# Kernel tuning notes

Measured on AMD Instinct MI355X. Metric: run time of the kernel, lower is better.

The kernel has to match this reference:

```python
import jax, jax.numpy as jnp
import numpy as np

CIN = 256
WINDOWS = (2, 4, 6)
LN_EPS = 1e-5


def _conv1x1(x, w, b):
    # x: (N,C,H,W), w: (O,C), b: (O,)
    return jnp.einsum('nchw,oc->nohw', x, w) + b[None, :, None, None]


def _pos_encoding(C, H, W):
    # Faithful to SinCosPositionalEncoding2D (incl. its w-major flatten + raw view)
    gw, gh = jnp.meshgrid(jnp.arange(W, dtype=jnp.float32),
                          jnp.arange(H, dtype=jnp.float32), indexing='ij')
    pd = C // 4
    omega = 1.0 / (10000.0 ** (jnp.arange(pd, dtype=jnp.float32) / pd))
    ow = gw.reshape(-1)[:, None] * omega[None, :]
    oh = gh.reshape(-1)[:, None] * omega[None, :]
    pe = jnp.concatenate([jnp.sin(ow), jnp.cos(ow), jnp.sin(oh), jnp.cos(oh)], axis=1)  # (W*H, C)
    return pe.reshape(1, C, H, W)  # raw row-major reinterpret, matching torch .view


def _unfold(x, kh, kw, sh, sw):
    # torch F.unfold semantics: (N,C,H,W) -> (N, C*kh*kw, L), L row-major over (oh, ow)
    N, C, H, W = x.shape
    oh = (H - kh) // sh + 1
    ow = (W - kw) // sw + 1
    ih = (jnp.arange(oh) * sh)[:, None] + jnp.arange(kh)[None, :]  # (oh,kh)
    iw = (jnp.arange(ow) * sw)[:, None] + jnp.arange(kw)[None, :]  # (ow,kw)
    p = x[:, :, ih[:, None, :, None], iw[None, :, None, :]]       # (N,C,oh,ow,kh,kw)
    return jnp.transpose(p, (0, 1, 4, 5, 2, 3)).reshape(N, C * kh * kw, oh * ow)


def _fold(p, H, W, kh, kw, sh, sw):
    # torch F.fold semantics: overlap-add scatter back to (N,C,H,W)
    N = p.shape[0]
    C = p.shape[1] // (kh * kw)
    oh = (H - kh) // sh + 1
    ow = (W - kw) // sw + 1
    p = jnp.transpose(p.reshape(N, C, kh, kw, oh, ow), (0, 1, 4, 5, 2, 3))  # (N,C,oh,ow,kh,kw)
    ih = (jnp.arange(oh) * sh)[:, None] + jnp.arange(kh)[None, :]
    iw = (jnp.arange(ow) * sw)[:, None] + jnp.arange(kw)[None, :]
    out = jnp.zeros((N, C, H, W), p.dtype)
    return out.at[:, :, ih[:, None, :, None], iw[None, :, None, :]].add(p)


def _psa(x, ch_wv_w, ch_wv_b, ch_wq_w, ch_wq_b, ch_wz_w, ch_wz_b, ln_g, ln_b,
         sp_wv_w, sp_wv_b, sp_wq_w, sp_wq_b):
    # Polarized Self-Attention (parallel), input (N,C,H',W')
    N, C, Hh, Ww = x.shape
    C2 = C // 2
    HW = Hh * Ww
    # channel-only branch
    wv = _conv1x1(x, ch_wv_w, ch_wv_b).reshape(N, C2, HW)
    wq = jax.nn.softmax(_conv1x1(x, ch_wq_w, ch_wq_b).reshape(N, HW), axis=-1)
    z = jnp.einsum('ncl,nl->nc', wv, wq)                       # (N, C2)
    wz = jnp.einsum('nc,oc->no', z, ch_wz_w) + ch_wz_b         # (N, C)
    m = wz.mean(-1, keepdims=True)
    v = ((wz - m) ** 2).mean(-1, keepdims=True)
    ch_w = jax.nn.sigmoid((wz - m) / jnp.sqrt(v + LN_EPS) * ln_g + ln_b)
    out_ch = x * ch_w[:, :, None, None]
    # spatial-only branch
    sv = _conv1x1(x, sp_wv_w, sp_wv_b).reshape(N, C2, HW)
    sq = jax.nn.softmax(_conv1x1(x, sp_wq_w, sp_wq_b).mean(axis=(2, 3)), axis=-1)  # (N,C2)
    sp_w = jax.nn.sigmoid(jnp.einsum('nc,ncl->nl', sq, sv)).reshape(N, 1, Hh, Ww)
    return out_ch + x * sp_w


def _forward(x, w_exp, b_exp, w_res, b_res, w_fus, b_fus,
             ch_wv_w, ch_wv_b, ch_wq_w, ch_wq_b, ch_wz_w, ch_wz_b, ln_g, ln_b,
             sp_wv_w, sp_wv_b, sp_wq_w, sp_wq_b):
    N, C, H, W = x.shape
    expx = _conv1x1(x, w_exp, b_exp)                 # (N, 3C, H, W)
    branches = jnp.split(expx, len(WINDOWS), axis=1)
    pos = _pos_encoding(C, H, W)
    outs = []
    for i, win in enumerate(WINDOWS):
        sh, sw = H // win, W // win
        kh, kw = sh + H % win, sw + W % win
        K = kh * kw
        u = _unfold(branches[i], kh, kw, sh, sw).reshape(N, C, win * win, K)
        pu = _unfold(pos, kh, kw, sh, sw).reshape(1, C, win * win, K)
        a = _psa(u + pu, ch_wv_w, ch_wv_b, ch_wq_w, ch_wq_b, ch_wz_w, ch_wz_b,
                 ln_g, ln_b, sp_wv_w, sp_wv_b, sp_wq_w, sp_wq_b)
        a = a.reshape(N, C * K, win * win)           # raw view, matching torch
        cnt = _fold(jnp.ones_like(a), H, W, kh, kw, sh, sw)
        f = _fold(a, H, W, kh, kw, sh, sw) / cnt
        outs.append(f)
    out = _conv1x1(jnp.concatenate(outs, axis=1) + expx, w_res, b_res) + x
    return _conv1x1(out, w_fus, b_fus)


def setup_inputs() -> dict:
    key = jax.random.key(0)
    ks = jax.random.split(key, 10)
    C, C2 = CIN, CIN // 2
    s = 0.02
    nrm = lambda k, shp: jax.random.normal(k, shp, jnp.float32) * s
    return {
        'x': jax.random.normal(ks[0], (8, C, 64, 64), jnp.float32),
        'w_exp': nrm(ks[1], (3 * C, C)), 'b_exp': jnp.zeros((3 * C,), jnp.float32),
        'w_res': nrm(ks[2], (C, 3 * C)), 'b_res': jnp.zeros((C,), jnp.float32),
        'w_fus': nrm(ks[3], (C, C)), 'b_fus': jnp.zeros((C,), jnp.float32),
        'ch_wv_w': nrm(ks[4], (C2, C)), 'ch_wv_b': jnp.zeros((C2,), jnp.float32),
        'ch_wq_w': nrm(ks[5], (1, C)), 'ch_wq_b': jnp.zeros((1,), jnp.float32),
        'ch_wz_w': nrm(ks[6], (C, C2)), 'ch_wz_b': jnp.zeros((C,), jnp.float32),
        'ln_g': jnp.ones((C,), jnp.float32), 'ln_b': jnp.zeros((C,), jnp.float32),
        'sp_wv_w': nrm(ks[7], (C2, C)), 'sp_wv_b': jnp.zeros((C2,), jnp.float32),
        'sp_wq_w': nrm(ks[8], (C2, C)), 'sp_wq_b': jnp.zeros((C2,), jnp.float32),
    }


def reference(x, w_exp, b_exp, w_res, b_res, w_fus, b_fus,
              ch_wv_w, ch_wv_b, ch_wq_w, ch_wq_b, ch_wz_w, ch_wz_b, ln_g, ln_b,
              sp_wv_w, sp_wv_b, sp_wq_w, sp_wq_b):
    return _forward(x, w_exp, b_exp, w_res, b_res, w_fus, b_fus,
                    ch_wv_w, ch_wv_b, ch_wq_w, ch_wq_b, ch_wz_w, ch_wz_b, ln_g, ln_b,
                    sp_wv_w, sp_wv_b, sp_wq_w, sp_wq_b)
```

## Files before the change

### kernel.cpp

```cpp
#include <hip/hip_runtime.h>
#include <cstddef>


#define HW 4096
typedef unsigned short ushort_t;
typedef __attribute__((ext_vector_type(8))) short bf16x8;
typedef __attribute__((ext_vector_type(4))) float floatx4;

__device__ __forceinline__ ushort_t f2bf(float f) {
    unsigned u = __float_as_uint(f);
    u += 0x7FFF + ((u >> 16) & 1);
    return (ushort_t)(u >> 16);
}
__device__ __forceinline__ float bf2f(ushort_t h) {
    return __uint_as_float(((unsigned)h) << 16);
}

__device__ __forceinline__ int cnt1f(int y, int sh, int kh, int win) {
    int t = y - kh + sh;
    int lo = t > 0 ? t / sh : 0;
    int hi = min(win - 1, y / sh);
    return hi - lo + 1;
}

__device__ __forceinline__ float posval(int f) {
    int row = f >> 8, col = f & 255;
    int a = row >> 6, b = row & 63;
    int g = col >> 6, k = col & 63;
    float omega = expf(-(float)k * (9.2103403719761836f / 64.f));
    float arg = (g < 2 ? (float)a : (float)b) * omega;
    return (g & 1) ? cosf(arg) : sinf(arg);
}

__global__ __launch_bounds__(256) void prep_all(
    const float* __restrict__ x, const float* __restrict__ W_exp,
    const float* __restrict__ b_exp, const float* __restrict__ wq,
    const float* __restrict__ wq_b, const float* __restrict__ W_fus,
    const float* __restrict__ W_res, const float* __restrict__ b_res,
    const float* __restrict__ b_fus,
    float* __restrict__ pos, float* __restrict__ posT,
    ushort_t* __restrict__ xbT, ushort_t* __restrict__ wexpb,
    float* __restrict__ g, float* __restrict__ c0out,
    ushort_t* __restrict__ Wcat, float* __restrict__ biasc,
    float* __restrict__ zeroreg)
{
    __shared__ float smf[1184];
    int b = blockIdx.x, tid = threadIdx.x;
    if (b < 4096) {
        int idx = b * 256 + tid;
        pos[idx] = posval(idx);
        int p = idx >> 8, c = idx & 255;
        posT[idx] = posval(c * 4096 + p);
    } else if (b < 12288) {
        int v = b - 4096;
        int p0 = (v & 127) * 32, c0 = ((v >> 7) & 7) * 32, n = v >> 10;
        int cc = tid >> 3, p4 = (tid & 7) * 4;
        const float* src = x + (((size_t)(n * 256 + c0 + cc)) << 12) + p0 + p4;
        float4 vv = *(const float4*)src;
        smf[cc * 37 + p4] = vv.x; smf[cc * 37 + p4 + 1] = vv.y;
        smf[cc * 37 + p4 + 2] = vv.z; smf[cc * 37 + p4 + 3] = vv.w;
        __syncthreads();
        int pp = tid >> 3, c4 = (tid & 7) * 4;
        unsigned lo = (unsigned)f2bf(smf[c4 * 37 + pp]) | ((unsigned)f2bf(smf[(c4 + 1) * 37 + pp]) << 16);
        unsigned hi = (unsigned)f2bf(smf[(c4 + 2) * 37 + pp]) | ((unsigned)f2bf(smf[(c4 + 3) * 37 + pp]) << 16);
        *(uint2*)&xbT[(((size_t)(n << 12)) + p0 + pp) * 256 + c0 + c4] = make_uint2(lo, hi);
    } else if (b < 13056) {
        int i = (b - 12288) * 256 + tid;
        wexpb[i] = f2bf(W_exp[i]);
    } else if (b < 13059) {
        int i = b - 13056;
        float* wql = smf;
        float* red = smf + 256;
        wql[tid] = wq[tid];
        red[tid] = wq[tid] * b_exp[i * 256 + tid];
        __syncthreads();
        const float* Wb = W_exp + ((size_t)(i * 256)) * 256 + tid;
        float acc = 0.f;
        #pragma unroll 8
        for (int oc = 0; oc < 256; ++oc) acc = fmaf(wql[oc], Wb[(size_t)oc * 256], acc);
        g[i * 256 + tid] = acc;
        for (int s = 128; s > 0; s >>= 1) { if (tid < s) red[tid] += red[tid + s]; __syncthreads(); }
        if (tid == 0) c0out[i] = red[0] + wq_b[0];
    } else if (b < 13827) {
        int v = b - 13059;
        int o = v & 255, jb = v >> 8;
        float* wrow = smf;
        float* red = smf + 256;
        wrow[tid] = W_fus[o * 256 + tid];
        __syncthreads();
        int j = jb * 256 + tid;
        float acc = 0.f;
        #pragma unroll 8
        for (int c = 0; c < 256; ++c) acc = fmaf(wrow[c], W_res[(size_t)c * 768 + j], acc);
        Wcat[o * 1024 + 256 + j] = f2bf(acc);
        if (jb == 0) {
            Wcat[o * 1024 + tid] = f2bf(wrow[tid]);
            red[tid] = wrow[tid] * b_res[tid];
            __syncthreads();
            for (int s = 128; s > 0; s >>= 1) { if (tid < s) red[tid] += red[tid + s]; __syncthreads(); }
            if (tid == 0) biasc[o] = red[0] + b_fus[o];
        }
    } else {
        int i = (b - 13827) * 256 + tid;
        zeroreg[i] = 0.f;
    }
}

__global__ __launch_bounds__(256) void xbar_kernel(
    const float* __restrict__ x, const float* __restrict__ pos,
    float* __restrict__ xbar_all, float* __restrict__ xbar6,
    float* __restrict__ posbar, float* __restrict__ posbar6)
{
    int c = blockIdx.x, n = blockIdx.y, tid = threadIdx.x;
    const float* src = (n < 8) ? x + (((size_t)(n * 256 + c)) << 12)
                               : pos + (((size_t)c) << 12);
    float sa = 0.f, s6 = 0.f;
    #pragma unroll
    for (int k = 0; k < 4; ++k) {
        int f4 = tid + k * 256;
        float4 v = *(const float4*)(src + f4 * 4);
        int p = f4 * 4;
        int y = p >> 6, xx = p & 63;
        float cy = (float)cnt1f(y, 10, 14, 6);
        float c0_ = cy * (float)cnt1f(xx + 0, 10, 14, 6);
        float c1_ = cy * (float)cnt1f(xx + 1, 10, 14, 6);
        float c2_ = cy * (float)cnt1f(xx + 2, 10, 14, 6);
        float c3_ = cy * (float)cnt1f(xx + 3, 10, 14, 6);
        sa += v.x + v.y + v.z + v.w;
        s6 += c0_ * v.x + c1_ * v.y + c2_ * v.z + c3_ * v.w;
    }
    __shared__ float red[256];
    red[tid] = sa; __syncthreads();
    for (int s = 128; s > 0; s >>= 1) { if (tid < s) red[tid] += red[tid + s]; __syncthreads(); }
    float ra = red[0]; __syncthreads();
    red[tid] = s6; __syncthreads();
    for (int s = 128; s > 0; s >>= 1) { if (tid < s) red[tid] += red[tid + s]; __syncthreads(); }
    float r6 = red[0];
    if (tid == 0) {
        if (n < 8) { xbar_all[n * 256 + c] = ra; xbar6[n * 256 + c] = r6; }
        else       { posbar[c] = ra;             posbar6[c] = r6; }
    }
}

__global__ __launch_bounds__(512) void qdot_ubar(
    const float* __restrict__ x, const float* __restrict__ pos,
    const float* __restrict__ g, const float* __restrict__ c0in,
    const float* __restrict__ wq, float* __restrict__ qdot,
    const float* __restrict__ W_exp, const float* __restrict__ b_exp,
    const float* __restrict__ xbar_all, const float* __restrict__ xbar6,
    const float* __restrict__ posbar, const float* __restrict__ posbar6,
    float* __restrict__ ubar)
{
    int blk = blockIdx.x, tid = threadIdx.x;
    if (blk < 256) {
        int n = blk >> 5;
        int ph = tid & 127, cq = tid >> 7;
        int p = (blk & 31) * 128 + ph;
        __shared__ float gl[768];
        __shared__ float wql[256];
        __shared__ float4 red4[512];
        for (int k = tid; k < 768; k += 512) gl[k] = g[k];
        if (tid < 256) wql[tid] = wq[tid];
        __syncthreads();
        const float* xp = x + (((size_t)n) << 20) + p;
        const float* pp = pos + p;
        float q0 = 0.f, q1 = 0.f, q2 = 0.f, qp = 0.f;
        #pragma unroll 4
        for (int c = cq * 64; c < cq * 64 + 64; ++c) {
            float xv = xp[(size_t)c << 12];
            float pv = pp[(size_t)c << 12];
            q0 = fmaf(gl[c], xv, q0);
            q1 = fmaf(gl[256 + c], xv, q1);
            q2 = fmaf(gl[512 + c], xv, q2);
            qp = fmaf(wql[c], pv, qp);
        }
        red4[tid] = make_float4(q0, q1, q2, qp);
        __syncthreads();
        if (tid < 128) {
            float4 a = red4[tid], b = red4[128 + tid], cc = red4[256 + tid], d = red4[384 + tid];
            float rp = a.w + b.w + cc.w + d.w;
            qdot[((0 * 8 + n) << 12) + p] = a.x + b.x + cc.x + d.x + rp + c0in[0];
            qdot[((1 * 8 + n) << 12) + p] = a.y + b.y + cc.y + d.y + rp + c0in[1];
            qdot[((2 * 8 + n) << 12) + p] = a.z + b.z + cc.z + d.z + rp + c0in[2];
        }
    } else {
        int v = blk - 256;
        int i = v >> 3, n = v & 7;
        __shared__ float xbl[256];
        if (tid < 256) xbl[tid] = ((i < 2) ? xbar_all : xbar6)[n * 256 + tid];
        __syncthreads();
        if (tid < 256) {
            int win = 2 * (i + 1), sh = 64 / win, kh = sh + 64 % win;
            float Li = (float)(win * win * kh * kh);
            float acc = b_exp[i * 256 + tid] * Li + ((i < 2) ? posbar : posbar6)[tid];
            const float* Wr = W_exp + ((size_t)(i * 256 + tid)) * 256;
            #pragma unroll 8
            for (int j = 0; j < 256; ++j) acc = fmaf(Wr[j], xbl[j], acc);
            ubar[(i * 8 + n) * 256 + tid] = acc;
        }
    }
}

__global__ __launch_bounds__(256) void pass_b_h(
    const float* __restrict__ qdot, const float* __restrict__ ubar_raw,
    const float* __restrict__ sp_wq_w, const float* __restrict__ sp_wq_b,
    const float* __restrict__ sp_wv_w, const float* __restrict__ sp_wv_b,
    const float* __restrict__ W_exp, const float* __restrict__ b_exp,
    float* __restrict__ Mn, float* __restrict__ invZn,
    float* __restrict__ w_eff, float* __restrict__ h, float* __restrict__ btot)
{
    int i = blockIdx.x, n = blockIdx.y, tid = threadIdx.x;
    int b = i * 8 + n;
    int win = 2 * (i + 1), sh = 64 / win, kh = sh + 64 % win;
    float invL = 1.f / (float)(win * win * kh * kh);
    const float* qd = qdot + (((size_t)b) << 12);
    __shared__ float red[256];
    __shared__ float ub[256];
    __shared__ float spq[128];
    __shared__ float we[256];
    float m = -1e30f;
    for (int p = tid; p < HW; p += 256) m = fmaxf(m, qd[p]);
    red[tid] = m; __syncthreads();
    for (int s = 128; s > 0; s >>= 1) { if (tid < s) red[tid] = fmaxf(red[tid], red[tid + s]); __syncthreads(); }
    float M = red[0]; __syncthreads();
    float z = 0.f;
    for (int p = tid; p < HW; p += 256) {
        int y = p >> 6, xx = p & 63;
        float cf = (float)(cnt1f(y, sh, kh, win) * cnt1f(xx, sh, kh, win));
        z += cf * expf(qd[p] - M);
    }
    red[tid] = z; __syncthreads();
    for (int s = 128; s > 0; s >>= 1) { if (tid < s) red[tid] += red[tid + s]; __syncthreads(); }
    float Z = red[0]; __syncthreads();
    if (tid == 0) { Mn[b] = M; invZn[b] = 1.f / Z; }
    ub[tid] = ubar_raw[b * 256 + tid] * invL;
    __syncthreads();
    float sl = -1e30f;
    if (tid < 128) {
        float a = sp_wq_b[tid];
        #pragma unroll 8
        for (int c = 0; c < 256; ++c) a = fmaf(sp_wq_w[tid * 256 + c], ub[c], a);
        sl = a;
    }
    red[tid] = sl; __syncthreads();
    for (int s = 128; s > 0; s >>= 1) { if (tid < s) red[tid] = fmaxf(red[tid], red[tid + s]); __syncthreads(); }
    float m2 = red[0]; __syncthreads();
    float e = (tid < 128) ? expf(sl - m2) : 0.f;
    red[tid] = e; __syncthreads();
    for (int s = 128; s > 0; s >>= 1) { if (tid < s) red[tid] += red[tid + s]; __syncthreads(); }
    float S2 = red[0]; __syncthreads();
    if (tid < 128) spq[tid] = e / S2;
    __syncthreads();
    float a = 0.f;
    #pragma unroll 8
    for (int c2 = 0; c2 < 128; ++c2) a = fmaf(spq[c2], sp_wv_w[c2 * 256 + tid], a);
    w_eff[b * 256 + tid] = a;
    we[tid] = a;
    red[tid] = (tid < 128) ? spq[tid] * sp_wv_b[tid] : 0.f;
    __syncthreads();
    for (int s = 128; s > 0; s >>= 1) { if (tid < s) red[tid] += red[tid + s]; __syncthreads(); }
    float beff = red[0]; __syncthreads();
    const float* Wb = W_exp + (size_t)i * 65536 + tid;
    float hacc = 0.f;
    #pragma unroll 8
    for (int oc = 0; oc < 256; ++oc) hacc = fmaf(we[oc], Wb[(size_t)oc * 256], hacc);
    h[b * 256 + tid] = hacc;
    red[tid] = we[tid] * b_exp[i * 256 + tid];
    __syncthreads();
    for (int s = 128; s > 0; s >>= 1) { if (tid < s) red[tid] += red[tid + s]; __syncthreads(); }
    if (tid == 0) btot[b] = red[0] + beff;
}

__global__ __launch_bounds__(512) void spw_t_xq(
    const float* __restrict__ x, const float* __restrict__ pos,
    const float* __restrict__ h, const float* __restrict__ weff,
    const float* __restrict__ qdot, const float* __restrict__ Mn,
    const float* __restrict__ invZn, const float* __restrict__ btot,
    const ushort_t* __restrict__ xbT, const float* __restrict__ posT,
    float* __restrict__ spw, float* __restrict__ xq, float* __restrict__ posq)
{
    int n = blockIdx.y, tid = threadIdx.x;
    int ph = tid & 127, cq = tid >> 7;
    int p0b = blockIdx.x * 128;
    int p = p0b + ph;
    __shared__ float hl[768], wl[768];
    __shared__ float4 red4[512];
    __shared__ float tl[3][128];
    for (int k = tid; k < 768; k += 512) {
        int i = k >> 8, c = k & 255;
        hl[k] = h[(i * 8 + n) * 256 + c];
        wl[k] = weff[(i * 8 + n) * 256 + c];
    }
    __syncthreads();
    const float* xp = x + (((size_t)n) << 20) + p;
    const float* pp = pos + p;
    float a0 = 0.f, a1 = 0.f, a2 = 0.f;
    #pragma unroll 4
    for (int c = cq * 64; c < cq * 64 + 64; ++c) {
        float xv = xp[(size_t)c << 12];
        float pv = pp[(size_t)c << 12];
        a0 += hl[c] * xv + wl[c] * pv;
        a1 += hl[256 + c] * xv + wl[256 + c] * pv;
        a2 += hl[512 + c] * xv + wl[512 + c] * pv;
    }
    red4[tid] = make_float4(a0, a1, a2, 0.f);
    __syncthreads();
    if (tid < 128) {
        float4 aa = red4[tid], bb = red4[128 + tid], cc = red4[256 + tid], dd = red4[384 + tid];
        float av[3] = {aa.x + bb.x + cc.x + dd.x,
                       aa.y + bb.y + cc.y + dd.y,
                       aa.z + bb.z + cc.z + dd.z};
        int y = p >> 6, xx = p & 63;
        #pragma unroll
        for (int i = 0; i < 3; ++i) {
            int b = i * 8 + n;
            int win = 2 * (i + 1), sh = 64 / win, kh = sh + 64 % win;
            float cf = (float)(cnt1f(y, sh, kh, win) * cnt1f(xx, sh, kh, win));
            int idx = (b << 12) + p;
            spw[idx] = 1.f / (1.f + expf(-(av[i] + btot[b])));
            tl[i][ph] = cf * expf(qdot[idx] - Mn[b]) * invZn[b];
        }
    }
    __syncthreads();
    int c = tid & 255;
    int half = tid >> 8;
    float s0 = 0.f, s1 = 0.f, s2 = 0.f;
    if (half == 0) {
        const ushort_t* xb = xbT + (((size_t)((n << 12) + p0b)) << 8) + c;
        #pragma unroll 4
        for (int pl = 0; pl < 128; ++pl) {
            float xv = bf2f(xb[(size_t)pl << 8]);
            s0 = fmaf(tl[0][pl], xv, s0);
            s1 = fmaf(tl[1][pl], xv, s1);
            s2 = fmaf(tl[2][pl], xv, s2);
        }
        atomicAdd(&xq[(0 * 8 + n) * 256 + c], s0);
        atomicAdd(&xq[(1 * 8 + n) * 256 + c], s1);
        atomicAdd(&xq[(2 * 8 + n) * 256 + c], s2);
    } else {
        const float* pt = posT + (((size_t)p0b) << 8) + c;
        #pragma unroll 4
        for (int pl = 0; pl < 128; ++pl) {
            float pv = pt[(size_t)pl << 8];
            s0 = fmaf(tl[0][pl], pv, s0);
            s1 = fmaf(tl[1][pl], pv, s1);
            s2 = fmaf(tl[2][pl], pv, s2);
        }
        atomicAdd(&posq[(0 * 8 + n) * 256 + c], s0);
        atomicAdd(&posq[(1 * 8 + n) * 256 + c], s1);
        atomicAdd(&posq[(2 * 8 + n) * 256 + c], s2);
    }
}

__global__ __launch_bounds__(256) void pass_d_uq(
    const float* __restrict__ W_exp, const float* __restrict__ b_exp,
    const float* __restrict__ xq, const float* __restrict__ posq,
    const float* __restrict__ ch_wv_w, const float* __restrict__ ch_wv_b,
    const float* __restrict__ ch_wz_w, const float* __restrict__ ch_wz_b,
    const float* __restrict__ ln_g, const float* __restrict__ ln_b,
    float* __restrict__ ch_w)
{
    int i = blockIdx.x, n = blockIdx.y, tid = threadIdx.x;
    int b = i * 8 + n;
    __shared__ float xql[256];
    __shared__ float uql[256];
    __shared__ float zz[128];
    __shared__ float red[256];
    xql[tid] = xq[b * 256 + tid];
    __syncthreads();
    float acc = b_exp[i * 256 + tid] + posq[b * 256 + tid];
    const float* Wr = W_exp + ((size_t)(i * 256 + tid)) * 256;
    #pragma unroll 8
    for (int cin = 0; cin < 256; ++cin) acc = fmaf(Wr[cin], xql[cin], acc);
    uql[tid] = acc;
    __syncthreads();
    if (tid < 128) {
        float a = ch_wv_b[tid];
        #pragma unroll 8
        for (int c = 0; c < 256; ++c) a = fmaf(ch_wv_w[tid * 256 + c], uql[c], a);
        zz[tid] = a;
    }
    __syncthreads();
    float wz = ch_wz_b[tid];
    #pragma unroll 8
    for (int c2 = 0; c2 < 128; ++c2) wz = fmaf(ch_wz_w[tid * 128 + c2], zz[c2], wz);
    red[tid] = wz; __syncthreads();
    for (int s = 128; s > 0; s >>= 1) { if (tid < s) red[tid] += red[tid + s]; __syncthreads(); }
    float mean = red[0] * (1.f / 256.f); __syncthreads();
    float d = wz - mean;
    red[tid] = d * d; __syncthreads();
    for (int s = 128; s > 0; s >>= 1) { if (tid < s) red[tid] += red[tid + s]; __syncthreads(); }
    float var = red[0] * (1.f / 256.f);
    float xn = d / sqrtf(var + 1e-5f);
    ch_w[b * 256 + tid] = 1.f / (1.f + expf(-(xn * ln_g[tid] + ln_b[tid])));
}

__global__ __launch_bounds__(256) void gemm_expT(
    const ushort_t* __restrict__ Wb, const ushort_t* __restrict__ XT,
    const float* __restrict__ bias, const float* __restrict__ posT,
    const float* __restrict__ chw, const float* __restrict__ spw,
    ushort_t* __restrict__ OutT)
{
    __shared__ ushort_t SM[10240];
    ushort_t* As = SM;
    ushort_t* Bs = SM + 5120;
    int n = blockIdx.z;
    int p0 = blockIdx.x * 128;
    int o0 = blockIdx.y * 128;
    int t = threadIdx.x;
    int lane = t & 63, wave = t >> 6;
    int wm = (wave & 1) * 64, wn = (wave >> 1) * 64;
    int lr = lane & 15, lk = (lane >> 4) * 8;
    int ar = t >> 2, ac = (t & 3) * 8;
    const ushort_t* A0 = Wb + (size_t)(o0 + ar) * 256 + ac;
    const ushort_t* A1 = Wb + (size_t)(o0 + ar + 64) * 256 + ac;
    const ushort_t* B0 = XT + (((size_t)(n << 12)) + p0 + ar) * 256 + ac;
    const ushort_t* B1 = XT + (((size_t)(n << 12)) + p0 + ar + 64) * 256 + ac;
    floatx4 acc[4][4] = {};
    for (int k0 = 0; k0 < 256; k0 += 32) {
        uint4 a0 = *(const uint4*)(A0 + k0);
        uint4 a1 = *(const uint4*)(A1 + k0);
        uint4 b0 = *(const uint4*)(B0 + k0);
        uint4 b1 = *(const uint4*)(B1 + k0);
        __syncthreads();
        *(uint4*)&As[ar * 40 + ac] = a0;
        *(uint4*)&As[(ar + 64) * 40 + ac] = a1;
        *(uint4*)&Bs[ar * 40 + ac] = b0;
        *(uint4*)&Bs[(ar + 64) * 40 + ac] = b1;
        __syncthreads();
        bf16x8 af[4], bfr[4];
        #pragma unroll
        for (int mi = 0; mi < 4; ++mi)
            af[mi] = *(const bf16x8*)&As[(wm + mi * 16 + lr) * 40 + lk];
        #pragma unroll
        for (int ni = 0; ni < 4; ++ni)
            bfr[ni] = *(const bf16x8*)&Bs[(wn + ni * 16 + lr) * 40 + lk];
        #pragma unroll
        for (int mi = 0; mi < 4; ++mi)
            #pragma unroll
            for (int ni = 0; ni < 4; ++ni)
                acc[mi][ni] = __builtin_amdgcn_mfma_f32_16x16x32_bf16(
                    af[mi], bfr[ni], acc[mi][ni], 0, 0, 0);
    }
    int col = lane & 15, rb = (lane >> 4) * 4;
    int ibr = o0 >> 8;
    int bi = ibr * 8 + n;
    #pragma unroll
    for (int r = 0; r < 2; ++r) {
        __syncthreads();
        if (wm == r * 64) {
            #pragma unroll
            for (int mi = 0; mi < 4; ++mi) {
                int o_loc = mi * 16 + rb;
                float4 bo = *(const float4*)&bias[o0 + r * 64 + o_loc];
                #pragma unroll
                for (int ni = 0; ni < 4; ++ni) {
                    int prow = wn + ni * 16 + col;
                    floatx4 v = acc[mi][ni];
                    unsigned lo = (unsigned)f2bf(v[0] + bo.x) | ((unsigned)f2bf(v[1] + bo.y) << 16);
                    unsigned hi = (unsigned)f2bf(v[2] + bo.z) | ((unsigned)f2bf(v[3] + bo.w) << 16);
                    *(uint2*)&SM[prow * 72 + o_loc] = make_uint2(lo, hi);
                }
            }
        }
        __syncthreads();
        #pragma unroll
        for (int it = 0; it < 4; ++it) {
            int slot = it * 256 + t;
            int pl = slot >> 3, j = (slot & 7) * 8;
            uint4 raw = *(const uint4*)&SM[pl * 72 + j];
            float e0 = bf2f((ushort_t)(raw.x & 0xFFFF)), e1 = bf2f((ushort_t)(raw.x >> 16));
            float e2 = bf2f((ushort_t)(raw.y & 0xFFFF)), e3 = bf2f((ushort_t)(raw.y >> 16));
            float e4 = bf2f((ushort_t)(raw.z & 0xFFFF)), e5 = bf2f((ushort_t)(raw.z >> 16));
            float e6 = bf2f((ushort_t)(raw.w & 0xFFFF)), e7 = bf2f((ushort_t)(raw.w >> 16));
            int p = p0 + pl;
            int cbase = (o0 & 255) + r * 64 + j;
            float s = spw[(bi << 12) + p];
            float4 q0 = *(const float4*)&posT[p * 256 + cbase];
            float4 q1 = *(const float4*)&posT[p * 256 + cbase + 4];
            float4 w0 = *(const float4*)&chw[bi * 256 + cbase];
            float4 w1 = *(const float4*)&chw[bi * 256 + cbase + 4];
            float r0 = e0 + (e0 + q0.x) * (w0.x + s);
            float r1 = e1 + (e1 + q0.y) * (w0.y + s);
            float r2 = e2 + (e2 + q0.z) * (w0.z + s);
            float r3 = e3 + (e3 + q0.w) * (w0.w + s);
            float r4 = e4 + (e4 + q1.x) * (w1.x + s);
            float r5 = e5 + (e5 + q1.y) * (w1.y + s);
            float r6 = e6 + (e6 + q1.z) * (w1.z + s);
            float r7 = e7 + (e7 + q1.w) * (w1.w + s);
            uint4 outv;
            outv.x = (unsigned)f2bf(r0) | ((unsigned)f2bf(r1) << 16);
            outv.y = (unsigned)f2bf(r2) | ((unsigned)f2bf(r3) << 16);
            outv.z = (unsigned)f2bf(r4) | ((unsigned)f2bf(r5) << 16);
            outv.w = (unsigned)f2bf(r6) | ((unsigned)f2bf(r7) << 16);
            *(uint4*)&OutT[(((size_t)(n << 12)) + p) * 768 + o0 + r * 64 + j] = outv;
        }
    }
}

__global__ __launch_bounds__(256) void gemm_out(
    const ushort_t* __restrict__ Wcat, const ushort_t* __restrict__ XT,
    const ushort_t* __restrict__ CT, const float* __restrict__ biasc,
    float* __restrict__ Out)
{
    __shared__ ushort_t As[128 * 40];
    __shared__ ushort_t Bs[128 * 40];
    int n = blockIdx.z;
    int p0 = blockIdx.x * 128;
    int o0 = blockIdx.y * 128;
    int t = threadIdx.x;
    int lane = t & 63, wave = t >> 6;
    int wm = (wave & 1) * 64, wn = (wave >> 1) * 64;
    int lr = lane & 15, lk = (lane >> 4) * 8;
    int ar = t >> 2, ac = (t & 3) * 8;
    const ushort_t* A0 = Wcat + (size_t)(o0 + ar) * 1024 + ac;
    const ushort_t* A1 = Wcat + (size_t)(o0 + ar + 64) * 1024 + ac;
    const ushort_t* BX0 = XT + (((size_t)(n << 12)) + p0 + ar) * 256 + ac;
    const ushort_t* BX1 = XT + (((size_t)(n << 12)) + p0 + ar + 64) * 256 + ac;
    const ushort_t* BC0 = CT + (((size_t)(n << 12)) + p0 + ar) * 768 + ac;
    const ushort_t* BC1 = CT + (((size_t)(n << 12)) + p0 + ar + 64) * 768 + ac;
    floatx4 acc[4][4] = {};
    for (int k0 = 0; k0 < 1024; k0 += 32) {
        const ushort_t* pb0 = (k0 < 256) ? (BX0 + k0) : (BC0 + (k0 - 256));
        const ushort_t* pb1 = (k0 < 256) ? (BX1 + k0) : (BC1 + (k0 - 256));
        uint4 a0 = *(const uint4*)(A0 + k0);
        uint4 a1 = *(const uint4*)(A1 + k0);
        uint4 b0 = *(const uint4*)pb0;
        uint4 b1 = *(const uint4*)pb1;
        __syncthreads();
        *(uint4*)&As[ar * 40 + ac] = a0;
        *(uint4*)&As[(ar + 64) * 40 + ac] = a1;
        *(uint4*)&Bs[ar * 40 + ac] = b0;
        *(uint4*)&Bs[(ar + 64) * 40 + ac] = b1;
        __syncthreads();
        bf16x8 af[4], bfr[4];
        #pragma unroll
        for (int mi = 0; mi < 4; ++mi)
            af[mi] = *(const bf16x8*)&As[(wm + mi * 16 + lr) * 40 + lk];
        #pragma unroll
        for (int ni = 0; ni < 4; ++ni)
            bfr[ni] = *(const bf16x8*)&Bs[(wn + ni * 16 + lr) * 40 + lk];
        #pragma unroll
        for (int mi = 0; mi < 4; ++mi)
            #pragma unroll
            for (int ni = 0; ni < 4; ++ni)
                acc[mi][ni] = __builtin_amdgcn_mfma_f32_16x16x32_bf16(
                    af[mi], bfr[ni], acc[mi][ni], 0, 0, 0);
    }
    int col = lane & 15, rb = (lane >> 4) * 4;
    #pragma unroll
    for (int mi = 0; mi < 4; ++mi) {
        int o = o0 + wm + mi * 16 + rb;
        float4 bo = *(const float4*)&biasc[o];
        #pragma unroll
        for (int r = 0; r < 4; ++r) {
            float br = (r == 0) ? bo.x : (r == 1) ? bo.y : (r == 2) ? bo.z : bo.w;
            #pragma unroll
            for (int ni = 0; ni < 4; ++ni) {
                int p = p0 + wn + ni * 16 + col;
                Out[(((size_t)(n * 256 + o + r)) << 12) + p] = acc[mi][ni][r] + br;
            }
        }
    }
}

extern "C" void kernel_launch(void* const* d_in, const int* in_sizes, int n_in,
                              void* d_out, int out_size, void* d_ws, size_t ws_size,
                              hipStream_t stream) {
    const float* x        = (const float*)d_in[0];
    const float* w_exp    = (const float*)d_in[1];
    const float* b_exp    = (const float*)d_in[2];
    const float* w_res    = (const float*)d_in[3];
    const float* b_res    = (const float*)d_in[4];
    const float* w_fus    = (const float*)d_in[5];
    const float* b_fus    = (const float*)d_in[6];
    const float* ch_wv_w  = (const float*)d_in[7];
    const float* ch_wv_b  = (const float*)d_in[8];
    const float* ch_wq_w  = (const float*)d_in[9];
    const float* ch_wq_b  = (const float*)d_in[10];
    const float* ch_wz_w  = (const float*)d_in[11];
    const float* ch_wz_b  = (const float*)d_in[12];
    const float* ln_g     = (const float*)d_in[13];
    const float* ln_b     = (const float*)d_in[14];
    const float* sp_wv_w  = (const float*)d_in[15];
    const float* sp_wv_b  = (const float*)d_in[16];
    const float* sp_wq_w  = (const float*)d_in[17];
    const float* sp_wq_b  = (const float*)d_in[18];
    float* out = (float*)d_out;
    float* ws  = (float*)d_ws;

    float*    pos   = ws + 0;
    float*    posT  = ws + 1048576;
    ushort_t* xbT   = (ushort_t*)(ws + 2097152);
    ushort_t* exT   = (ushort_t*)(ws + 6291456);
    ushort_t* wexpb = (ushort_t*)(ws + 18874368);
    ushort_t* Wcat  = (ushort_t*)(ws + 18972672);
    float*    qdot  = ws + 19103744;
    float*    spw   = ws + 19300352;
    float*    g     = ws + 19398656;
    float*    c0v   = ws + 19399424;
    float*    ubar  = ws + 19399428;
    float*    xba   = ws + 19405572;
    float*    xb6   = ws + 19407620;
    float*    pba   = ws + 19409668;
    float*    pb6   = ws + 19409924;
    float*    Mn    = ws + 19410180;
    float*    iZ    = ws + 19410204;
    float*    weff  = ws + 19410228;
    float*    btot  = ws + 19416372;
    float*    hb    = ws + 19416396;
    float*    xq    = ws + 19422540;
    float*    posq  = ws + 19428684;
    float*    chw   = ws + 19434828;
    float*    biasc = ws + 19440972;

    prep_all<<<13875, 256, 0, stream>>>(x, w_exp, b_exp, ch_wq_w, ch_wq_b,
                                        w_fus, w_res, b_res, b_fus,
                                        pos, posT, xbT, wexpb, g, c0v,
                                        Wcat, biasc, xq);
    xbar_kernel<<<dim3(256, 9), 256, 0, stream>>>(x, pos, xba, xb6, pba, pb6);
    qdot_ubar<<<280, 512, 0, stream>>>(x, pos, g, c0v, ch_wq_w, qdot,
                                       w_exp, b_exp, xba, xb6, pba, pb6, ubar);
    pass_b_h<<<dim3(3, 8), 256, 0, stream>>>(qdot, ubar, sp_wq_w, sp_wq_b,
                                             sp_wv_w, sp_wv_b, w_exp, b_exp,
                                             Mn, iZ, weff, hb, btot);
    spw_t_xq<<<dim3(32, 8), 512, 0, stream>>>(x, pos, hb, weff, qdot, Mn, iZ,
                                              btot, xbT, posT, spw, xq, posq);
    pass_d_uq<<<dim3(3, 8), 256, 0, stream>>>(w_exp, b_exp, xq, posq,
                                              ch_wv_w, ch_wv_b, ch_wz_w, ch_wz_b,
                                              ln_g, ln_b, chw);
    gemm_expT<<<dim3(32, 6, 8), 256, 0, stream>>>(wexpb, xbT, b_exp, posT, chw, spw, exT);
    gemm_out<<<dim3(32, 2, 8), 256, 0, stream>>>(Wcat, xbT, exT, biasc, out);
}
```

Measured before the change: 293.9 us.

## Fuse spatial sums into prep, transpose small weights, double-buffer GEMMs via direct LDS loads

Removes the separate xbar kernel and computes per-block partial sums of x and pos, plain and window-count-weighted, inside prep_all. qdot_ubar then reduces those partials. The weight matrices used by the small matvec kernels are pre-transposed so their per-thread loops read coalesced columns. Both bf16 MFMA GEMMs now stage tiles with global_load_lds into double-buffered shared memory, overlapping the next tile's load with compute and dropping one barrier per step. The cost is extra workspace, more prep blocks, and an unpadded LDS layout that may cause bank conflicts.

```diff
diff --git a/kernel.cpp b/kernel.cpp
--- a/kernel.cpp
+++ b/kernel.cpp
@@ -1,5 +1,6 @@
 #include <hip/hip_runtime.h>
 #include <cstddef>
+#include <cstdint>
 
 
 #define HW 4096
@@ -32,31 +33,72 @@
     return (g & 1) ? cosf(arg) : sinf(arg);
 }
 
+__device__ __forceinline__ void gload16(const ushort_t* g, ushort_t* l) {
+    const __attribute__((address_space(1))) unsigned int* gp =
+        reinterpret_cast<const __attribute__((address_space(1))) unsigned int*>(
+            reinterpret_cast<uintptr_t>(g));
+    __attribute__((address_space(3))) unsigned int* lp =
+        reinterpret_cast<__attribute__((address_space(3))) unsigned int*>(
+            reinterpret_cast<uintptr_t>(l));
+    __builtin_amdgcn_global_load_lds(gp, lp, 16, 0, 0);
+}
+
 __global__ __launch_bounds__(256) void prep_all(
     const float* __restrict__ x, const float* __restrict__ W_exp,
     const float* __restrict__ b_exp, const float* __restrict__ wq,
     const float* __restrict__ wq_b, const float* __restrict__ W_fus,
     const float* __restrict__ W_res, const float* __restrict__ b_res,
-    const float* __restrict__ b_fus,
+    const float* __restrict__ b_fus, const float* __restrict__ sp_wq_w,
+    const float* __restrict__ ch_wv_w, const float* __restrict__ ch_wz_w,
     float* __restrict__ pos, float* __restrict__ posT,
     ushort_t* __restrict__ xbT, ushort_t* __restrict__ wexpb,
     float* __restrict__ g, float* __restrict__ c0out,
     ushort_t* __restrict__ Wcat, float* __restrict__ biasc,
-    float* __restrict__ zeroreg)
+    float* __restrict__ zeroreg,
+    float* __restrict__ W_expT, float* __restrict__ swqT,
+    float* __restrict__ chvT, float* __restrict__ chzT,
+    float* __restrict__ xpa, float* __restrict__ xp6,
+    float* __restrict__ ppa, float* __restrict__ pp6)
 {
     __shared__ float smf[1184];
+    __shared__ float pr[256];
+    __shared__ float pr6[256];
     int b = blockIdx.x, tid = threadIdx.x;
     if (b < 4096) {
         int idx = b * 256 + tid;
-        pos[idx] = posval(idx);
-        int p = idx >> 8, c = idx & 255;
-        posT[idx] = posval(c * 4096 + p);
+        float pv = posval(idx);
+        pos[idx] = pv;
+        int p2 = idx >> 8, c2 = idx & 255;
+        posT[idx] = posval(c2 * 4096 + p2);
+        int p = ((b & 15) << 8) + tid;
+        int y = p >> 6, xx = p & 63;
+        float cf = (float)(cnt1f(y, 10, 14, 6) * cnt1f(xx, 10, 14, 6));
+        smf[tid] = pv; smf[256 + tid] = cf * pv;
+        __syncthreads();
+        for (int s = 128; s > 0; s >>= 1) {
+            if (tid < s) { smf[tid] += smf[tid + s]; smf[256 + tid] += smf[256 + tid + s]; }
+            __syncthreads();
+        }
+        if (tid == 0) {
+            int slot = (b & 15) * 256 + (b >> 4);
+            ppa[slot] = smf[0];
+            pp6[slot] = smf[256];
+        }
     } else if (b < 12288) {
         int v = b - 4096;
         int p0 = (v & 127) * 32, c0 = ((v >> 7) & 7) * 32, n = v >> 10;
         int cc = tid >> 3, p4 = (tid & 7) * 4;
         const float* src = x + (((size_t)(n * 256 + c0 + cc)) << 12) + p0 + p4;
         float4 vv = *(const float4*)src;
+        int pg = p0 + p4;
+        int y = pg >> 6, xx = pg & 63;
+        float cy = (float)cnt1f(y, 10, 14, 6);
+        float s6 = cy * ((float)cnt1f(xx, 10, 14, 6) * vv.x
+                       + (float)cnt1f(xx + 1, 10, 14, 6) * vv.y
+                       + (float)cnt1f(xx + 2, 10, 14, 6) * vv.z
+                       + (float)cnt1f(xx + 3, 10, 14, 6) * vv.w);
+        pr[tid] = vv.x + vv.y + vv.z + vv.w;
+        pr6[tid] = s6;
         smf[cc * 37 + p4] = vv.x; smf[cc * 37 + p4 + 1] = vv.y;
         smf[cc * 37 + p4 + 2] = vv.z; smf[cc * 37 + p4 + 3] = vv.w;
         __syncthreads();
@@ -64,6 +106,14 @@
         unsigned lo = (unsigned)f2bf(smf[c4 * 37 + pp]) | ((unsigned)f2bf(smf[(c4 + 1) * 37 + pp]) << 16);
         unsigned hi = (unsigned)f2bf(smf[(c4 + 2) * 37 + pp]) | ((unsigned)f2bf(smf[(c4 + 3) * 37 + pp]) << 16);
         *(uint2*)&xbT[(((size_t)(n << 12)) + p0 + pp) * 256 + c0 + c4] = make_uint2(lo, hi);
+        if (tid < 32) {
+            float s = 0.f, s66 = 0.f;
+            #pragma unroll
+            for (int k = 0; k < 8; ++k) { s += pr[tid * 8 + k]; s66 += pr6[tid * 8 + k]; }
+            int pblk = v & 127;
+            xpa[pblk * 2048 + n * 256 + c0 + tid] = s;
+            xp6[pblk * 2048 + n * 256 + c0 + tid] = s66;
+        }
     } else if (b < 13056) {
         int i = (b - 12288) * 256 + tid;
         wexpb[i] = f2bf(W_exp[i]);
@@ -100,45 +150,21 @@
             for (int s = 128; s > 0; s >>= 1) { if (tid < s) red[tid] += red[tid + s]; __syncthreads(); }
             if (tid == 0) biasc[o] = red[0] + b_fus[o];
         }
-    } else {
+    } else if (b < 13875) {
         int i = (b - 13827) * 256 + tid;
         zeroreg[i] = 0.f;
-    }
-}
-
-__global__ __launch_bounds__(256) void xbar_kernel(
-    const float* __restrict__ x, const float* __restrict__ pos,
-    float* __restrict__ xbar_all, float* __restrict__ xbar6,
-    float* __restrict__ posbar, float* __restrict__ posbar6)
-{
-    int c = blockIdx.x, n = blockIdx.y, tid = threadIdx.x;
-    const float* src = (n < 8) ? x + (((size_t)(n * 256 + c)) << 12)
-                               : pos + (((size_t)c) << 12);
-    float sa = 0.f, s6 = 0.f;
-    #pragma unroll
-    for (int k = 0; k < 4; ++k) {
-        int f4 = tid + k * 256;
-        float4 v = *(const float4*)(src + f4 * 4);
-        int p = f4 * 4;
-        int y = p >> 6, xx = p & 63;
-        float cy = (float)cnt1f(y, 10, 14, 6);
-        float c0_ = cy * (float)cnt1f(xx + 0, 10, 14, 6);
-        float c1_ = cy * (float)cnt1f(xx + 1, 10, 14, 6);
-        float c2_ = cy * (float)cnt1f(xx + 2, 10, 14, 6);
-        float c3_ = cy * (float)cnt1f(xx + 3, 10, 14, 6);
-        sa += v.x + v.y + v.z + v.w;
-        s6 += c0_ * v.x + c1_ * v.y + c2_ * v.z + c3_ * v.w;
-    }
-    __shared__ float red[256];
-    red[tid] = sa; __syncthreads();
-    for (int s = 128; s > 0; s >>= 1) { if (tid < s) red[tid] += red[tid + s]; __syncthreads(); }
-    float ra = red[0]; __syncthreads();
-    red[tid] = s6; __syncthreads();
-    for (int s = 128; s > 0; s >>= 1) { if (tid < s) red[tid] += red[tid + s]; __syncthreads(); }
-    float r6 = red[0];
-    if (tid == 0) {
-        if (n < 8) { xbar_all[n * 256 + c] = ra; xbar6[n * 256 + c] = r6; }
-        else       { posbar[c] = ra;             posbar6[c] = r6; }
+    } else if (b < 14643) {
+        int idx = (b - 13875) * 256 + tid;
+        W_expT[(idx & 255) * 768 + (idx >> 8)] = W_exp[idx];
+    } else if (b < 14771) {
+        int idx = (b - 14643) * 256 + tid;
+        swqT[(idx & 255) * 128 + (idx >> 8)] = sp_wq_w[idx];
+    } else if (b < 14899) {
+        int idx = (b - 14771) * 256 + tid;
+        chvT[(idx & 255) * 128 + (idx >> 8)] = ch_wv_w[idx];
+    } else {
+        int idx = (b - 14899) * 256 + tid;
+        chzT[(idx & 127) * 256 + (idx >> 7)] = ch_wz_w[idx];
     }
 }
 
@@ -146,10 +172,10 @@
     const float* __restrict__ x, const float* __restrict__ pos,
     const float* __restrict__ g, const float* __restrict__ c0in,
     const float* __restrict__ wq, float* __restrict__ qdot,
-    const float* __restrict__ W_exp, const float* __restrict__ b_exp,
-    const float* __restrict__ xbar_all, const float* __restrict__ xbar6,
-    const float* __restrict__ posbar, const float* __restrict__ posbar6,
-    float* __restrict__ ubar)
+    const float* __restrict__ b_exp,
+    const float* __restrict__ xpa, const float* __restrict__ xp6,
+    const float* __restrict__ ppa, const float* __restrict__ pp6,
+    const float* __restrict__ W_expT, float* __restrict__ ubar)
 {
     int blk = blockIdx.x, tid = threadIdx.x;
     if (blk < 256) {
@@ -187,15 +213,25 @@
         int v = blk - 256;
         int i = v >> 3, n = v & 7;
         __shared__ float xbl[256];
-        if (tid < 256) xbl[tid] = ((i < 2) ? xbar_all : xbar6)[n * 256 + tid];
-        __syncthreads();
         if (tid < 256) {
+            const float* xp_ = (i < 2) ? xpa : xp6;
+            float s = 0.f;
+            #pragma unroll 8
+            for (int k = 0; k < 128; ++k) s += xp_[k * 2048 + n * 256 + tid];
+            xbl[tid] = s;
+        }
+        __syncthreads();
+        if (tid < 256) {
+            const float* pp_ = (i < 2) ? ppa : pp6;
+            float pb = 0.f;
+            #pragma unroll
+            for (int k = 0; k < 16; ++k) pb += pp_[k * 256 + tid];
             int win = 2 * (i + 1), sh = 64 / win, kh = sh + 64 % win;
             float Li = (float)(win * win * kh * kh);
-            float acc = b_exp[i * 256 + tid] * Li + ((i < 2) ? posbar : posbar6)[tid];
-            const float* Wr = W_exp + ((size_t)(i * 256 + tid)) * 256;
+            float acc = b_exp[i * 256 + tid] * Li + pb;
+            const float* Wc = W_expT + i * 256 + tid;
             #pragma unroll 8
-            for (int j = 0; j < 256; ++j) acc = fmaf(Wr[j], xbl[j], acc);
+            for (int j = 0; j < 256; ++j) acc = fmaf(Wc[(size_t)j * 768], xbl[j], acc);
             ubar[(i * 8 + n) * 256 + tid] = acc;
         }
     }
@@ -203,7 +239,7 @@
 
 __global__ __launch_bounds__(256) void pass_b_h(
     const float* __restrict__ qdot, const float* __restrict__ ubar_raw,
-    const float* __restrict__ sp_wq_w, const float* __restrict__ sp_wq_b,
+    const float* __restrict__ swqT, const float* __restrict__ sp_wq_b,
     const float* __restrict__ sp_wv_w, const float* __restrict__ sp_wv_b,
     const float* __restrict__ W_exp, const float* __restrict__ b_exp,
     float* __restrict__ Mn, float* __restrict__ invZn,
@@ -239,7 +275,7 @@
     if (tid < 128) {
         float a = sp_wq_b[tid];
         #pragma unroll 8
-        for (int c = 0; c < 256; ++c) a = fmaf(sp_wq_w[tid * 256 + c], ub[c], a);
+        for (int c = 0; c < 256; ++c) a = fmaf(swqT[c * 128 + tid], ub[c], a);
         sl = a;
     }
     red[tid] = sl; __syncthreads();
@@ -353,10 +389,10 @@
 }
 
 __global__ __launch_bounds__(256) void pass_d_uq(
-    const float* __restrict__ W_exp, const float* __restrict__ b_exp,
+    const float* __restrict__ W_expT, const float* __restrict__ b_exp,
     const float* __restrict__ xq, const float* __restrict__ posq,
-    const float* __restrict__ ch_wv_w, const float* __restrict__ ch_wv_b,
-    const float* __restrict__ ch_wz_w, const float* __restrict__ ch_wz_b,
+    const float* __restrict__ chvT, const float* __restrict__ ch_wv_b,
+    const float* __restrict__ chzT, const float* __restrict__ ch_wz_b,
     const float* __restrict__ ln_g, const float* __restrict__ ln_b,
     float* __restrict__ ch_w)
 {
@@ -369,21 +405,21 @@
     xql[tid] = xq[b * 256 + tid];
     __syncthreads();
     float acc = b_exp[i * 256 + tid] + posq[b * 256 + tid];
-    const float* Wr = W_exp + ((size_t)(i * 256 + tid)) * 256;
+    const float* Wc = W_expT + i * 256 + tid;
     #pragma unroll 8
-    for (int cin = 0; cin < 256; ++cin) acc = fmaf(Wr[cin], xql[cin], acc);
+    for (int cin = 0; cin < 256; ++cin) acc = fmaf(Wc[(size_t)cin * 768], xql[cin], acc);
     uql[tid] = acc;
     __syncthreads();
     if (tid < 128) {
         float a = ch_wv_b[tid];
         #pragma unroll 8
-        for (int c = 0; c < 256; ++c) a = fmaf(ch_wv_w[tid * 256 + c], uql[c], a);
+        for (int c = 0; c < 256; ++c) a = fmaf(chvT[c * 128 + tid], uql[c], a);
         zz[tid] = a;
     }
     __syncthreads();
     float wz = ch_wz_b[tid];
     #pragma unroll 8
-    for (int c2 = 0; c2 < 128; ++c2) wz = fmaf(ch_wz_w[tid * 128 + c2], zz[c2], wz);
+    for (int c2 = 0; c2 < 128; ++c2) wz = fmaf(chzT[c2 * 256 + tid], zz[c2], wz);
     red[tid] = wz; __syncthreads();
     for (int s = 128; s > 0; s >>= 1) { if (tid < s) red[tid] += red[tid + s]; __syncthreads(); }
     float mean = red[0] * (1.f / 256.f); __syncthreads();
@@ -401,46 +437,47 @@
     const float* __restrict__ chw, const float* __restrict__ spw,
     ushort_t* __restrict__ OutT)
 {
-    __shared__ ushort_t SM[10240];
-    ushort_t* As = SM;
-    ushort_t* Bs = SM + 5120;
+    __shared__ __align__(16) ushort_t SM[16384];
     int n = blockIdx.z;
     int p0 = blockIdx.x * 128;
     int o0 = blockIdx.y * 128;
     int t = threadIdx.x;
     int lane = t & 63, wave = t >> 6;
     int wm = (wave & 1) * 64, wn = (wave >> 1) * 64;
-    int lr = lane & 15, lk = (lane >> 4) * 8;
-    int ar = t >> 2, ac = (t & 3) * 8;
-    const ushort_t* A0 = Wb + (size_t)(o0 + ar) * 256 + ac;
-    const ushort_t* A1 = Wb + (size_t)(o0 + ar + 64) * 256 + ac;
-    const ushort_t* B0 = XT + (((size_t)(n << 12)) + p0 + ar) * 256 + ac;
-    const ushort_t* B1 = XT + (((size_t)(n << 12)) + p0 + ar + 64) * 256 + ac;
+    int lr = lane & 15;
+    int srow = (wave & 1) * 64 + lane;
+    int scol = (wave >> 1) * 8;
+    const ushort_t* gA = Wb + (size_t)(o0 + srow) * 256 + scol;
+    const ushort_t* gB = XT + (((size_t)(n << 12)) + p0 + srow) * 256 + scol;
+    auto stage = [&](int buf, int k0a) {
+        ushort_t* base = &SM[buf * 8192 + wave * 512];
+        gload16(gA + k0a,      base);
+        gload16(gA + k0a + 16, base + 2048);
+        gload16(gB + k0a,      base + 4096);
+        gload16(gB + k0a + 16, base + 6144);
+    };
     floatx4 acc[4][4] = {};
+    stage(0, 0);
+    __syncthreads();
+    int cur = 0;
     for (int k0 = 0; k0 < 256; k0 += 32) {
-        uint4 a0 = *(const uint4*)(A0 + k0);
-        uint4 a1 = *(const uint4*)(A1 + k0);
-        uint4 b0 = *(const uint4*)(B0 + k0);
-        uint4 b1 = *(const uint4*)(B1 + k0);
-        __syncthreads();
-        *(uint4*)&As[ar * 40 + ac] = a0;
-        *(uint4*)&As[(ar + 64) * 40 + ac] = a1;
-        *(uint4*)&Bs[ar * 40 + ac] = b0;
-        *(uint4*)&Bs[(ar + 64) * 40 + ac] = b1;
-        __syncthreads();
+        if (k0 + 32 < 256) stage(cur ^ 1, k0 + 32);
+        int fb = cur * 8192 + ((lane >> 4) << 10);
         bf16x8 af[4], bfr[4];
         #pragma unroll
         for (int mi = 0; mi < 4; ++mi)
-            af[mi] = *(const bf16x8*)&As[(wm + mi * 16 + lr) * 40 + lk];
+            af[mi] = *(const bf16x8*)&SM[fb + (wm + mi * 16 + lr) * 8];
         #pragma unroll
         for (int ni = 0; ni < 4; ++ni)
-            bfr[ni] = *(const bf16x8*)&Bs[(wn + ni * 16 + lr) * 40 + lk];
+            bfr[ni] = *(const bf16x8*)&SM[fb + 4096 + (wn + ni * 16 + lr) * 8];
         #pragma unroll
         for (int mi = 0; mi < 4; ++mi)
             #pragma unroll
             for (int ni = 0; ni < 4; ++ni)
                 acc[mi][ni] = __builtin_amdgcn_mfma_f32_16x16x32_bf16(
                     af[mi], bfr[ni], acc[mi][ni], 0, 0, 0);
+        __syncthreads();
+        cur ^= 1;
     }
     int col = lane & 15, rb = (lane >> 4) * 4;
     int ibr = o0 >> 8;
@@ -503,49 +540,49 @@
     const ushort_t* __restrict__ CT, const float* __restrict__ biasc,
     float* __restrict__ Out)
 {
-    __shared__ ushort_t As[128 * 40];
-    __shared__ ushort_t Bs[128 * 40];
+    __shared__ __align__(16) ushort_t SM[16384];
     int n = blockIdx.z;
     int p0 = blockIdx.x * 128;
     int o0 = blockIdx.y * 128;
     int t = threadIdx.x;
     int lane = t & 63, wave = t >> 6;
     int wm = (wave & 1) * 64, wn = (wave >> 1) * 64;
-    int lr = lane & 15, lk = (lane >> 4) * 8;
-    int ar = t >> 2, ac = (t & 3) * 8;
-    const ushort_t* A0 = Wcat + (size_t)(o0 + ar) * 1024 + ac;
-    const ushort_t* A1 = Wcat + (size_t)(o0 + ar + 64) * 1024 + ac;
-    const ushort_t* BX0 = XT + (((size_t)(n << 12)) + p0 + ar) * 256 + ac;
-    const ushort_t* BX1 = XT + (((size_t)(n << 12)) + p0 + ar + 64) * 256 + ac;
-    const ushort_t* BC0 = CT + (((size_t)(n << 12)) + p0 + ar) * 768 + ac;
-    const ushort_t* BC1 = CT + (((size_t)(n << 12)) + p0 + ar + 64) * 768 + ac;
+    int lr = lane & 15;
+    int srow = (wave & 1) * 64 + lane;
+    int scol = (wave >> 1) * 8;
+    const ushort_t* gA  = Wcat + (size_t)(o0 + srow) * 1024 + scol;
+    const ushort_t* gBX = XT + (((size_t)(n << 12)) + p0 + srow) * 256 + scol;
+    const ushort_t* gBC = CT + (((size_t)(n << 12)) + p0 + srow) * 768 + scol;
+    auto stage = [&](int buf, int k0a) {
+        ushort_t* base = &SM[buf * 8192 + wave * 512];
+        const ushort_t* pb = (k0a < 256) ? (gBX + k0a) : (gBC + (k0a - 256));
+        gload16(gA + k0a,      base);
+        gload16(gA + k0a + 16, base + 2048);
+        gload16(pb,            base + 4096);
+        gload16(pb + 16,       base + 6144);
+    };
     floatx4 acc[4][4] = {};
+    stage(0, 0);
+    __syncthreads();
+    int cur = 0;
     for (int k0 = 0; k0 < 1024; k0 += 32) {
-        const ushort_t* pb0 = (k0 < 256) ? (BX0 + k0) : (BC0 + (k0 - 256));
-        const ushort_t* pb1 = (k0 < 256) ? (BX1 + k0) : (BC1 + (k0 - 256));
-        uint4 a0 = *(const uint4*)(A0 + k0);
-        uint4 a1 = *(const uint4*)(A1 + k0);
-        uint4 b0 = *(const uint4*)pb0;
-        uint4 b1 = *(const uint4*)pb1;
-        __syncthreads();
-        *(uint4*)&As[ar * 40 + ac] = a0;
-        *(uint4*)&As[(ar + 64) * 40 + ac] = a1;
-        *(uint4*)&Bs[ar * 40 + ac] = b0;
-        *(uint4*)&Bs[(ar + 64) * 40 + ac] = b1;
-        __syncthreads();
+        if (k0 + 32 < 1024) stage(cur ^ 1, k0 + 32);
+        int fb = cur * 8192 + ((lane >> 4) << 10);
         bf16x8 af[4], bfr[4];
         #pragma unroll
         for (int mi = 0; mi < 4; ++mi)
-            af[mi] = *(const bf16x8*)&As[(wm + mi * 16 + lr) * 40 + lk];
+            af[mi] = *(const bf16x8*)&SM[fb + (wm + mi * 16 + lr) * 8];
         #pragma unroll
         for (int ni = 0; ni < 4; ++ni)
-            bfr[ni] = *(const bf16x8*)&Bs[(wn + ni * 16 + lr) * 40 + lk];
+            bfr[ni] = *(const bf16x8*)&SM[fb + 4096 + (wn + ni * 16 + lr) * 8];
         #pragma unroll
         for (int mi = 0; mi < 4; ++mi)
             #pragma unroll
             for (int ni = 0; ni < 4; ++ni)
                 acc[mi][ni] = __builtin_amdgcn_mfma_f32_16x16x32_bf16(
                     af[mi], bfr[ni], acc[mi][ni], 0, 0, 0);
+        __syncthreads();
+        cur ^= 1;
     }
     int col = lane & 15, rb = (lane >> 4) * 4;
     #pragma unroll
@@ -600,10 +637,6 @@
     float*    g     = ws + 19398656;
     float*    c0v   = ws + 19399424;
     float*    ubar  = ws + 19399428;
-    float*    xba   = ws + 19405572;
-    float*    xb6   = ws + 19407620;
-    float*    pba   = ws + 19409668;
-    float*    pb6   = ws + 19409924;
     float*    Mn    = ws + 19410180;
     float*    iZ    = ws + 19410204;
     float*    weff  = ws + 19410228;
@@ -613,21 +646,31 @@
     float*    posq  = ws + 19428684;
     float*    chw   = ws + 19434828;
     float*    biasc = ws + 19440972;
-
-    prep_all<<<13875, 256, 0, stream>>>(x, w_exp, b_exp, ch_wq_w, ch_wq_b,
+    float*    W_expT = ws + 19441228;
+    float*    swqT   = ws + 19637836;
+    float*    chvT   = ws + 19670604;
+    float*    chzT   = ws + 19703372;
+    float*    xpa    = ws + 19736140;
+    float*    xp6    = ws + 19998284;
+    float*    ppa    = ws + 20260428;
+    float*    pp6    = ws + 20264524;
+
+    prep_all<<<15027, 256, 0, stream>>>(x, w_exp, b_exp, ch_wq_w, ch_wq_b,
                                         w_fus, w_res, b_res, b_fus,
+                                        sp_wq_w, ch_wv_w, ch_wz_w,
                                         pos, posT, xbT, wexpb, g, c0v,
-                                        Wcat, biasc, xq);
-    xbar_kernel<<<dim3(256, 9), 256, 0, stream>>>(x, pos, xba, xb6, pba, pb6);
+                                        Wcat, biasc, xq,
+                                        W_expT, swqT, chvT, chzT,
+                                        xpa, xp6, ppa, pp6);
     qdot_ubar<<<280, 512, 0, stream>>>(x, pos, g, c0v, ch_wq_w, qdot,
-                                       w_exp, b_exp, xba, xb6, pba, pb6, ubar);
-    pass_b_h<<<dim3(3, 8), 256, 0, stream>>>(qdot, ubar, sp_wq_w, sp_wq_b,
+                                       b_exp, xpa, xp6, ppa, pp6, W_expT, ubar);
+    pass_b_h<<<dim3(3, 8), 256, 0, stream>>>(qdot, ubar, swqT, sp_wq_b,
                                              sp_wv_w, sp_wv_b, w_exp, b_exp,
                                              Mn, iZ, weff, hb, btot);
     spw_t_xq<<<dim3(32, 8), 512, 0, stream>>>(x, pos, hb, weff, qdot, Mn, iZ,
                                               btot, xbT, posT, spw, xq, posq);
-    pass_d_uq<<<dim3(3, 8), 256, 0, stream>>>(w_exp, b_exp, xq, posq,
-                                              ch_wv_w, ch_wv_b, ch_wz_w, ch_wz_b,
+    pass_d_uq<<<dim3(3, 8), 256, 0, stream>>>(W_expT, b_exp, xq, posq,
+                                              chvT, ch_wv_b, chzT, ch_wz_b,
                                               ln_g, ln_b, chw);
     gemm_expT<<<dim3(32, 6, 8), 256, 0, stream>>>(wexpb, xbT, b_exp, posT, chw, spw, exT);
     gemm_out<<<dim3(32, 2, 8), 256, 0, stream>>>(Wcat, xbT, exT, biasc, out);
```

Result: slower. 319.1 us (+8.6%).
